# Performance work log

Measured on AMD Instinct MI355X. Metric: run time of the kernel, lower is better.

The kernel has to match this reference:

```python
import jax, jax.numpy as jnp
import numpy as np

HEADS = 16
EPS = 1e-5  # nn.LayerNorm default


def setup_inputs() -> dict:
    key = jax.random.key(0)
    ks = jax.random.split(key, 3)
    b, n, dim = 4, 1024, 1024
    x = jax.random.normal(ks[0], (b, n, dim), jnp.float32)
    ln_gamma = jnp.ones((dim,), jnp.float32)
    ln_beta = jnp.zeros((dim,), jnp.float32)
    # torch.nn.Linear stores weight as [out_features, in_features]
    w_qkv = jax.random.normal(ks[1], (3 * dim, dim), jnp.float32) * (dim ** -0.5)
    w_out = jax.random.normal(ks[2], (dim, dim), jnp.float32) * (dim ** -0.5)
    b_out = jnp.zeros((dim,), jnp.float32)
    return {"x": x, "ln_gamma": ln_gamma, "ln_beta": ln_beta,
            "w_qkv": w_qkv, "w_out": w_out, "b_out": b_out, "topk": 32}


def reference(x, ln_gamma, ln_beta, w_qkv, w_out, b_out, topk):
    b, n, dim = x.shape
    h = HEADS
    d = dim // h
    scale = d ** -0.5  # (inner_dim/heads)^-0.5 with inner_dim=dim

    # LayerNorm (biased variance, matching torch)
    mu = x.mean(-1, keepdims=True)
    var = x.var(-1, keepdims=True)
    xn = (x - mu) * jax.lax.rsqrt(var + EPS) * ln_gamma + ln_beta

    # qkv projection (no bias): y = x @ W^T
    qkv = jnp.einsum('bnd,ed->bne', xn, w_qkv)  # [b, n, 3*dim]
    q, k, v = jnp.split(qkv, 3, axis=-1)
    split_heads = lambda t: t.reshape(b, n, h, d).transpose(0, 2, 1, 3)  # [b,h,n,d]
    q = split_heads(q) * scale
    k = split_heads(k)
    v = split_heads(v)

    sim = jnp.einsum('bhid,bhjd->bhij', q, k)          # [b,h,n,n]
    attn = jax.nn.softmax(sim, axis=-1)
    # top-k SELECTION: probability values are discarded, only indices used
    _, idx = jax.lax.top_k(attn, topk)                 # [b,h,n,topk]
    # gather v rows at top-k indices and sum (unweighted), matching
    # torch.gather(vv, 2, idx).sum(-2)
    gathered = jnp.take_along_axis(
        v, idx.reshape(b, h, n * topk)[..., None], axis=2)  # [b,h,n*topk,d]
    xsum = gathered.reshape(b, h, n, topk, d).sum(axis=3)   # [b,h,n,d]

    # global min/max normalization then exp
    xmin = xsum.min()
    xmax = xsum.max()
    out = jnp.exp((xsum - xmin) / (xmax - xmin))

    out = out.transpose(0, 2, 1, 3).reshape(b, n, dim)  # b h n d -> b n (h d)
    # final projection (self.out Linear; Dropout(0.2) inert at eval)
    return jnp.einsum('bnd,ed->bne', out, w_out) + b_out
```

## Files before the change

kernel.cpp:

```cpp
#include <hip/hip_runtime.h>


#define LN_EPS 1e-5f

using half8   = __attribute__((ext_vector_type(8))) _Float16;
using half4   = __attribute__((ext_vector_type(4))) _Float16;
using float4v = __attribute__((ext_vector_type(4))) float;

__device__ __forceinline__ void gload_lds16(const void* g, void* l) {
  __builtin_amdgcn_global_load_lds(
      (const __attribute__((address_space(1))) void*)g,
      (__attribute__((address_space(3))) void*)l, 16, 0, 0);
}
__device__ __forceinline__ float4v mfma16(half8 a, half8 b, float4v c) {
  return __builtin_amdgcn_mfma_f32_16x16x32_f16(a, b, c, 0, 0, 0);
}
struct HL { _Float16 h, l; };
__device__ __forceinline__ HL split2(float x) {
  _Float16 h = (_Float16)x;
  return { h, (_Float16)(x - (float)h) };
}

__device__ __forceinline__ unsigned fkey(float f) {
  unsigned u = __float_as_uint(f);
  return ((int)u < 0) ? ~u : (u | 0x80000000u);
}
__device__ __forceinline__ int enc_i(float f) {
  int i = __float_as_int(f);
  return i >= 0 ? i : (i ^ 0x7fffffff);
}
__device__ __forceinline__ float dec_i(int e) {
  return __int_as_float(e >= 0 ? e : (e ^ 0x7fffffff));
}

__global__ __launch_bounds__(256)
void ln_kernel(const float* __restrict__ x, const float* __restrict__ gamma,
               const float* __restrict__ beta,
               _Float16* __restrict__ xh, _Float16* __restrict__ xl) {
  __shared__ float red[8];
  int row = blockIdx.x, t = threadIdx.x;
  const float4* xr = (const float4*)(x + (size_t)row * 1024);
  float4 v = xr[t];
  float s  = v.x + v.y + v.z + v.w;
  float s2 = v.x*v.x + v.y*v.y + v.z*v.z + v.w*v.w;
  #pragma unroll
  for (int o = 32; o >= 1; o >>= 1) {
    s  += __shfl_xor(s,  o, 64);
    s2 += __shfl_xor(s2, o, 64);
  }
  int w = t >> 6, l = t & 63;
  if (l == 0) { red[w*2] = s; red[w*2+1] = s2; }
  __syncthreads();
  float S  = red[0] + red[2] + red[4] + red[6];
  float S2 = red[1] + red[3] + red[5] + red[7];
  float mu  = S * (1.0f/1024.0f);
  float var = S2 * (1.0f/1024.0f) - mu*mu;
  float r = rsqrtf(var + LN_EPS);
  float4 g  = ((const float4*)gamma)[t];
  float4 bb = ((const float4*)beta)[t];
  float o0 = (v.x - mu) * r * g.x + bb.x;
  float o1 = (v.y - mu) * r * g.y + bb.y;
  float o2 = (v.z - mu) * r * g.z + bb.z;
  float o3 = (v.w - mu) * r * g.w + bb.w;
  HL r0 = split2(o0), r1 = split2(o1), r2 = split2(o2), r3 = split2(o3);
  half4 hh = { r0.h, r1.h, r2.h, r3.h };
  half4 ll = { r0.l, r1.l, r2.l, r3.l };
  size_t e = (size_t)row * 1024 + t*4;
  *(half4*)(xh + e) = hh;
  *(half4*)(xl + e) = ll;
}

__global__ __launch_bounds__(256)
void cvt_kernel(const float* __restrict__ wqkv, const float* __restrict__ wout,
                _Float16* __restrict__ wqh, _Float16* __restrict__ wql,
                _Float16* __restrict__ woh, _Float16* __restrict__ wol) {
  size_t i4 = (size_t)blockIdx.x * 256 + threadIdx.x;
  const float* src; _Float16 *dh, *dl; size_t off;
  if (i4 < 786432) { src = wqkv; dh = wqh; dl = wql; off = i4; }
  else             { src = wout; dh = woh; dl = wol; off = i4 - 786432; }
  float4 v = ((const float4*)src)[off];
  HL r0 = split2(v.x), r1 = split2(v.y), r2 = split2(v.z), r3 = split2(v.w);
  half4 hh = { r0.h, r1.h, r2.h, r3.h };
  half4 ll = { r0.l, r1.l, r2.l, r3.l };
  ((half4*)dh)[off] = hh;
  ((half4*)dl)[off] = ll;
}

template<int MODE>
__global__ __launch_bounds__(256)
void gemm_f16split(const _Float16* __restrict__ Ah, const _Float16* __restrict__ Al,
                   const _Float16* __restrict__ Bh, const _Float16* __restrict__ Bl,
                   const float* __restrict__ bias, float* __restrict__ CO,
                   _Float16* __restrict__ QH, _Float16* __restrict__ QL,
                   _Float16* __restrict__ KH, _Float16* __restrict__ KL,
                   float* __restrict__ CV) {
  __shared__ __align__(16) _Float16 lds[4 * 128 * 32];
  const int K = 1024;
  int tid = threadIdx.x, w = tid >> 6, l = tid & 63;
  int m0 = blockIdx.y * 128, n0 = blockIdx.x * 128;
  int wm = (w >> 1) * 64, wn = (w & 1) * 64;

  const _Float16* src = (w == 0) ? Ah : (w == 1) ? Al : (w == 2) ? Bh : Bl;
  int rowbase = (w < 2) ? m0 : n0;
  _Float16* dst = lds + (size_t)w * 4096;
  int sr = l >> 2, sc = l & 3;

  float4v acc[4][4];
  #pragma unroll
  for (int u = 0; u < 4; ++u)
    #pragma unroll
    for (int vv = 0; vv < 4; ++vv) acc[u][vv] = (float4v){0.f, 0.f, 0.f, 0.f};

  int quad = l >> 4, lo16 = l & 15;
  for (int kt = 0; kt < K; kt += 32) {
    __syncthreads();
    #pragma unroll
    for (int i = 0; i < 8; ++i) {
      int row = i * 16 + sr;
      gload_lds16(src + (size_t)(rowbase + row) * K + kt + sc * 8,
                  dst + row * 32 + sc * 8);
    }
    __syncthreads();
    half8 ah[4], al[4], bh[4], bl[4];
    #pragma unroll
    for (int u = 0; u < 4; ++u) {
      int mrow = wm + u * 16 + lo16;
      int nrow = wn + u * 16 + lo16;
      ah[u] = *(const half8*)&lds[        (size_t)mrow * 32 + quad * 8];
      al[u] = *(const half8*)&lds[ 4096 + (size_t)mrow * 32 + quad * 8];
      bh[u] = *(const half8*)&lds[ 8192 + (size_t)nrow * 32 + quad * 8];
      bl[u] = *(const half8*)&lds[12288 + (size_t)nrow * 32 + quad * 8];
    }
    #pragma unroll
    for (int u = 0; u < 4; ++u)
      #pragma unroll
      for (int vv = 0; vv < 4; ++vv) {
        acc[u][vv] = mfma16(ah[u], bh[vv], acc[u][vv]);
        acc[u][vv] = mfma16(ah[u], bl[vv], acc[u][vv]);
        acc[u][vv] = mfma16(al[u], bh[vv], acc[u][vv]);
      }
  }

  #pragma unroll
  for (int u = 0; u < 4; ++u) {
    #pragma unroll
    for (int vv = 0; vv < 4; ++vv) {
      #pragma unroll
      for (int rg = 0; rg < 4; ++rg) {
        int row = m0 + wm + u * 16 + quad * 4 + rg;
        int col = n0 + wn + vv * 16 + lo16;
        float val = acc[u][vv][rg];
        if (MODE == 0) {
          int which = col >> 10, h = (col >> 6) & 15, dd = col & 63;
          int b = row >> 10, i = row & 1023;
          size_t e = ((size_t)(b * 16 + h) << 16) + ((size_t)i << 6) + dd;
          if (which == 2) { CV[e] = val; }
          else {
            HL sp = split2(val);
            if (which == 0) { QH[e] = sp.h; QL[e] = sp.l; }
            else            { KH[e] = sp.h; KL[e] = sp.l; }
          }
        } else {
          CO[(size_t)row * 1024 + col] = val + bias[col];
        }
      }
    }
  }
}

__global__ void init_kernel(int* minmax) {
  minmax[0] = 0x7fffffff;
  minmax[1] = (int)0x80000000;
}

__global__ __launch_bounds__(1024)
void attn_kernel(const _Float16* __restrict__ qh, const _Float16* __restrict__ ql,
                 const _Float16* __restrict__ kh, const _Float16* __restrict__ kl,
                 const float* __restrict__ vg, float* __restrict__ xsum) {
  __shared__ float simb[16][1028];
  __shared__ int sel[16][32];
  int g = blockIdx.x;
  int xcd = g & 7, slot = g >> 3;
  int bh = (slot >> 6) * 8 + xcd, grp = slot & 63;
  int tid = threadIdx.x, w = tid >> 6, l = tid & 63;
  int quad = l >> 4, lo16 = l & 15;
  size_t hb = (size_t)bh << 16;

  const _Float16* qhp = qh + hb + ((size_t)(grp * 16 + lo16) << 6);
  const _Float16* qlp = ql + hb + ((size_t)(grp * 16 + lo16) << 6);
  half8 ah0 = *(const half8*)(qhp + quad * 8);
  half8 ah1 = *(const half8*)(qhp + 32 + quad * 8);
  half8 al0 = *(const half8*)(qlp + quad * 8);
  half8 al1 = *(const half8*)(qlp + 32 + quad * 8);

  const _Float16* khp = kh + hb;
  const _Float16* klp = kl + hb;
  int jbase = w * 64;

  #pragma unroll
  for (int tt = 0; tt < 4; ++tt) {
    size_t off = ((size_t)(jbase + tt * 16 + lo16) << 6) + quad * 8;
    half8 b0 = *(const half8*)(khp + off);
    half8 b1 = *(const half8*)(khp + off + 32);
    half8 c0 = *(const half8*)(klp + off);
    half8 c1 = *(const half8*)(klp + off + 32);
    float4v acc = (float4v){0.f, 0.f, 0.f, 0.f};
    acc = mfma16(ah0, b0, acc);
    acc = mfma16(ah0, c0, acc);
    acc = mfma16(al0, b0, acc);
    acc = mfma16(ah1, b1, acc);
    acc = mfma16(ah1, c1, acc);
    acc = mfma16(al1, b1, acc);
    int jc = jbase + tt * 16 + lo16;
    #pragma unroll
    for (int rg = 0; rg < 4; ++rg)
      simb[quad * 4 + rg][jc] = acc[rg];
  }
  __syncthreads();

  unsigned long long below = (1ull << l) - 1ull;
  unsigned ku[16];
  #pragma unroll
  for (int s = 0; s < 16; ++s) ku[s] = fkey(simb[w][s * 64 + l]);

  unsigned cur = 0u;
  bool exact = false;
  for (int bit = 31; bit >= 0; --bit) {
    unsigned T = cur | (1u << bit);
    int c = 0;
    #pragma unroll
    for (int s = 0; s < 16; ++s) c += __popcll(__ballot(ku[s] >= T));
    if (c >= 32) {
      cur = T;
      if (c == 32) { exact = true; break; }
    }
  }
  int need = 9999;
  if (!exact) {
    int gcnt = 0;
    #pragma unroll
    for (int s = 0; s < 16; ++s) gcnt += __popcll(__ballot(ku[s] > cur));
    need = 32 - gcnt;
  }

  int base = 0, eqb = 0;
  #pragma unroll
  for (int s = 0; s < 16; ++s) {
    bool gt = ku[s] > cur;
    bool eq = ku[s] == cur;
    unsigned long long meq = __ballot(eq);
    int eqr = eqb + __popcll(meq & below);
    bool take = gt || (eq && (eqr < need));
    unsigned long long mtk = __ballot(take);
    if (take) sel[w][base + __popcll(mtk & below)] = s * 64 + l;
    base += __popcll(mtk);
    eqb  += __popcll(meq);
  }

  const float* vb = vg + hb;
  float acc = 0.0f;
  #pragma unroll
  for (int s2 = 0; s2 < 32; ++s2) {
    int j = sel[w][s2];
    acc += vb[((size_t)j << 6) + l];
  }
  xsum[hb + ((size_t)(grp * 16 + w) << 6) + l] = acc;
}

__global__ __launch_bounds__(256)
void reduce_kernel(const float* __restrict__ xsum, int* __restrict__ minmax) {
  __shared__ float red[8];
  int tid = threadIdx.x, w = tid >> 6, l = tid & 63;
  const float4* p = (const float4*)xsum + (size_t)blockIdx.x * 4096 + tid;
  float mn = 3.4e38f, mx = -3.4e38f;
  #pragma unroll
  for (int i = 0; i < 16; ++i) {
    float4 v = p[(size_t)i * 256];
    mn = fminf(mn, fminf(fminf(v.x, v.y), fminf(v.z, v.w)));
    mx = fmaxf(mx, fmaxf(fmaxf(v.x, v.y), fmaxf(v.z, v.w)));
  }
  #pragma unroll
  for (int o = 32; o >= 1; o >>= 1) {
    mn = fminf(mn, __shfl_xor(mn, o, 64));
    mx = fmaxf(mx, __shfl_xor(mx, o, 64));
  }
  if (l == 0) { red[w*2] = mn; red[w*2+1] = mx; }
  __syncthreads();
  if (tid == 0) {
    mn = fminf(fminf(red[0], red[2]), fminf(red[4], red[6]));
    mx = fmaxf(fmaxf(red[1], red[3]), fmaxf(red[5], red[7]));
    atomicMin(minmax,     enc_i(mn));
    atomicMax(minmax + 1, enc_i(mx));
  }
}

__global__ __launch_bounds__(256)
void fin_kernel(const float* __restrict__ xsum, const int* __restrict__ minmax,
                _Float16* __restrict__ oh, _Float16* __restrict__ ol) {
  int idx = blockIdx.x * 256 + threadIdx.x;
  float mn = dec_i(minmax[0]);
  float mx = dec_i(minmax[1]);
  float inv = 1.0f / (mx - mn);
  float4 xv = ((const float4*)xsum)[idx];
  float o0 = expf((xv.x - mn) * inv);
  float o1 = expf((xv.y - mn) * inv);
  float o2 = expf((xv.z - mn) * inv);
  float o3 = expf((xv.w - mn) * inv);
  HL r0 = split2(o0), r1 = split2(o1), r2 = split2(o2), r3 = split2(o3);
  half4 hh = { r0.h, r1.h, r2.h, r3.h };
  half4 ll = { r0.l, r1.l, r2.l, r3.l };
  int e0 = idx << 2;
  int bh = e0 >> 16, i = (e0 >> 6) & 1023, dd = e0 & 63;
  int b = bh >> 4, h = bh & 15;
  size_t oe = ((size_t)(b * 1024 + i) << 10) + (h << 6) + dd;
  *(half4*)(oh + oe) = hh;
  *(half4*)(ol + oe) = ll;
}

extern "C" void kernel_launch(void* const* d_in, const int* in_sizes, int n_in,
                              void* d_out, int out_size, void* d_ws, size_t ws_size,
                              hipStream_t stream) {
  const float* x     = (const float*)d_in[0];
  const float* gamma = (const float*)d_in[1];
  const float* beta  = (const float*)d_in[2];
  const float* w_qkv = (const float*)d_in[3];
  const float* w_out = (const float*)d_in[4];
  const float* b_out = (const float*)d_in[5];

  char* B = (char*)d_ws;
  const size_t MB = 1024ull * 1024ull;
  float*    v   = (float*)B;
  _Float16* qh  = (_Float16*)(B + 16*MB);
  _Float16* ql  = (_Float16*)(B + 24*MB);
  _Float16* kh  = (_Float16*)(B + 32*MB);
  _Float16* kl  = (_Float16*)(B + 40*MB);
  float*    xs  = (float*)(B + 48*MB);
  _Float16* xh  = (_Float16*)(B + 48*MB);
  _Float16* xl  = (_Float16*)(B + 56*MB);
  _Float16* woh = (_Float16*)(B + 64*MB);
  _Float16* wol = (_Float16*)(B + 66*MB);
  int*   minmax = (int*)(B + 68*MB);
  _Float16* wqh = (_Float16*)(B + 69*MB);
  _Float16* wql = (_Float16*)(B + 75*MB);
  _Float16* oth = qh;
  _Float16* otl = ql;

  ln_kernel<<<4096, 256, 0, stream>>>(x, gamma, beta, xh, xl);
  cvt_kernel<<<4096, 256, 0, stream>>>(w_qkv, w_out, wqh, wql, woh, wol);
  gemm_f16split<0><<<dim3(24, 32), 256, 0, stream>>>(
      xh, xl, wqh, wql, nullptr, nullptr, qh, ql, kh, kl, v);
  init_kernel<<<1, 1, 0, stream>>>(minmax);
  attn_kernel<<<4096, 1024, 0, stream>>>(qh, ql, kh, kl, v, xs);
  reduce_kernel<<<256, 256, 0, stream>>>(xs, minmax);
  fin_kernel<<<4096, 256, 0, stream>>>(xs, minmax, oth, otl);
  gemm_f16split<1><<<dim3(8, 32), 256, 0, stream>>>(
      oth, otl, woh, wol, b_out, (float*)d_out,
      nullptr, nullptr, nullptr, nullptr, nullptr);
}
```

Before: 427.3 us.

## Prefilter top-k candidates with mean+1.5σ threshold; vectorize V gather

Before the bitwise radix search for the top-32 threshold, each wavefront computes the row mean and variance of the scores and uses mean+1.5·std as a pre-threshold. If 32 to 128 candidates pass, it compacts them into LDS and runs the radix search over only two registers per lane instead of sixteen. Otherwise it falls back to the original full search, so the result stays exact. The V gather-sum is also changed to float4 loads spread across lane quarters with a shuffle reduction. This adds statistics work, extra branches and an extra LDS buffer.

```diff
diff --git a/kernel.cpp b/kernel.cpp
--- a/kernel.cpp
+++ b/kernel.cpp
@@ -179,6 +179,7 @@
                  const float* __restrict__ vg, float* __restrict__ xsum) {
   __shared__ float simb[16][1028];
   __shared__ int sel[16][32];
+  __shared__ unsigned short candj[16][128];
   int g = blockIdx.x;
   int xcd = g & 7, slot = g >> 3;
   int bh = (slot >> 6) * 8 + xcd, grp = slot & 63;
@@ -219,52 +220,143 @@
   __syncthreads();
 
   unsigned long long below = (1ull << l) - 1ull;
+  float s1 = 0.f, s2 = 0.f;
   unsigned ku[16];
   #pragma unroll
-  for (int s = 0; s < 16; ++s) ku[s] = fkey(simb[w][s * 64 + l]);
-
-  unsigned cur = 0u;
-  bool exact = false;
-  for (int bit = 31; bit >= 0; --bit) {
-    unsigned T = cur | (1u << bit);
-    int c = 0;
-    #pragma unroll
-    for (int s = 0; s < 16; ++s) c += __popcll(__ballot(ku[s] >= T));
-    if (c >= 32) {
-      cur = T;
-      if (c == 32) { exact = true; break; }
-    }
-  }
-  int need = 9999;
-  if (!exact) {
-    int gcnt = 0;
-    #pragma unroll
-    for (int s = 0; s < 16; ++s) gcnt += __popcll(__ballot(ku[s] > cur));
-    need = 32 - gcnt;
-  }
-
-  int base = 0, eqb = 0;
-  #pragma unroll
   for (int s = 0; s < 16; ++s) {
-    bool gt = ku[s] > cur;
-    bool eq = ku[s] == cur;
-    unsigned long long meq = __ballot(eq);
-    int eqr = eqb + __popcll(meq & below);
-    bool take = gt || (eq && (eqr < need));
-    unsigned long long mtk = __ballot(take);
-    if (take) sel[w][base + __popcll(mtk & below)] = s * 64 + l;
-    base += __popcll(mtk);
-    eqb  += __popcll(meq);
+    float fv = simb[w][s * 64 + l];
+    s1 += fv;
+    s2 += fv * fv;
+    ku[s] = fkey(fv);
+  }
+  #pragma unroll
+  for (int o = 32; o >= 1; o >>= 1) {
+    s1 += __shfl_xor(s1, o, 64);
+    s2 += __shfl_xor(s2, o, 64);
+  }
+  float mhat = s1 * (1.0f / 1024.0f);
+  float var  = s2 * (1.0f / 1024.0f) - mhat * mhat;
+  float T0f  = mhat + 1.5f * sqrtf(fmaxf(var, 0.f));
+  unsigned kT0 = fkey(T0f);
+
+  int C0 = 0;
+  bool ok = (T0f > 0.f);
+  unsigned long long msk[16];
+  if (ok) {
+    #pragma unroll
+    for (int s = 0; s < 16; ++s) {
+      msk[s] = __ballot(ku[s] >= kT0);
+      C0 += __popcll(msk[s]);
+    }
+    ok = (C0 >= 32 && C0 <= 128);
+  }
+
+  if (ok) {
+    int A = 0;
+    #pragma unroll
+    for (int s = 0; s < 16; ++s) {
+      bool a = (ku[s] >= kT0);
+      int r = A + __popcll(msk[s] & below);
+      if (a) candj[w][r] = (unsigned short)(s * 64 + l);
+      A += __popcll(msk[s]);
+    }
+    unsigned ck0 = 0u, ck1 = 0u;
+    int j0 = 0, j1 = 0;
+    if (l < A)      { j0 = candj[w][l];      ck0 = fkey(simb[w][j0]); }
+    if (64 + l < A) { j1 = candj[w][64 + l]; ck1 = fkey(simb[w][j1]); }
+
+    unsigned cur; int need;
+    if (C0 == 32) {
+      cur = kT0; need = 9999;
+    } else {
+      cur = 0u; bool exact = false;
+      for (int bit = 31; bit >= 0; --bit) {
+        unsigned T = cur | (1u << bit);
+        if (T <= kT0) { cur = T; continue; }
+        int c = __popcll(__ballot(ck0 >= T)) + __popcll(__ballot(ck1 >= T));
+        if (c >= 32) {
+          cur = T;
+          if (c == 32) { exact = true; break; }
+        }
+      }
+      if (exact) need = 9999;
+      else {
+        int gcnt = __popcll(__ballot(ck0 > cur)) + __popcll(__ballot(ck1 > cur));
+        need = 32 - gcnt;
+      }
+    }
+    int base = 0, eqb = 0;
+    {
+      bool gt = ck0 > cur, eq = ck0 == cur;
+      unsigned long long meq = __ballot(eq);
+      int eqr = eqb + __popcll(meq & below);
+      bool take = gt || (eq && (eqr < need));
+      unsigned long long mtk = __ballot(take);
+      if (take) sel[w][base + __popcll(mtk & below)] = j0;
+      base += __popcll(mtk);
+      eqb  += __popcll(meq);
+    }
+    {
+      bool gt = ck1 > cur, eq = ck1 == cur;
+      unsigned long long meq = __ballot(eq);
+      int eqr = eqb + __popcll(meq & below);
+      bool take = gt || (eq && (eqr < need));
+      unsigned long long mtk = __ballot(take);
+      if (take) sel[w][base + __popcll(mtk & below)] = j1;
+      base += __popcll(mtk);
+      eqb  += __popcll(meq);
+    }
+  } else {
+    unsigned cur = 0u; bool exact = false;
+    for (int bit = 31; bit >= 0; --bit) {
+      unsigned T = cur | (1u << bit);
+      int c = 0;
+      #pragma unroll
+      for (int s = 0; s < 16; ++s) c += __popcll(__ballot(ku[s] >= T));
+      if (c >= 32) {
+        cur = T;
+        if (c == 32) { exact = true; break; }
+      }
+    }
+    int need = 9999;
+    if (!exact) {
+      int gcnt = 0;
+      #pragma unroll
+      for (int s = 0; s < 16; ++s) gcnt += __popcll(__ballot(ku[s] > cur));
+      need = 32 - gcnt;
+    }
+    int base = 0, eqb = 0;
+    #pragma unroll
+    for (int s = 0; s < 16; ++s) {
+      bool gt = ku[s] > cur;
+      bool eq = ku[s] == cur;
+      unsigned long long meq = __ballot(eq);
+      int eqr = eqb + __popcll(meq & below);
+      bool take = gt || (eq && (eqr < need));
+      unsigned long long mtk = __ballot(take);
+      if (take) sel[w][base + __popcll(mtk & below)] = s * 64 + l;
+      base += __popcll(mtk);
+      eqb  += __popcll(meq);
+    }
   }
 
   const float* vb = vg + hb;
-  float acc = 0.0f;
-  #pragma unroll
-  for (int s2 = 0; s2 < 32; ++s2) {
-    int j = sel[w][s2];
-    acc += vb[((size_t)j << 6) + l];
-  }
-  xsum[hb + ((size_t)(grp * 16 + w) << 6) + l] = acc;
+  float4 vacc = {0.f, 0.f, 0.f, 0.f};
+  #pragma unroll
+  for (int p = 0; p < 8; ++p) {
+    int j = sel[w][p * 4 + (l >> 4)];
+    float4 t = *(const float4*)(vb + ((size_t)j << 6) + (l & 15) * 4);
+    vacc.x += t.x; vacc.y += t.y; vacc.z += t.z; vacc.w += t.w;
+  }
+  #pragma unroll
+  for (int o = 32; o >= 16; o >>= 1) {
+    vacc.x += __shfl_xor(vacc.x, o, 64);
+    vacc.y += __shfl_xor(vacc.y, o, 64);
+    vacc.z += __shfl_xor(vacc.z, o, 64);
+    vacc.w += __shfl_xor(vacc.w, o, 64);
+  }
+  if (l < 16)
+    *(float4*)(xsum + hb + ((size_t)(grp * 16 + w) << 6) + l * 4) = vacc;
 }
 
 __global__ __launch_bounds__(256)
```

Result: slower. 479.3 us (+12.2%).
